# Kernel tuning notes

Measured on AMD Instinct MI355X. Metric: run time of the kernel, lower is better.

The kernel has to match this reference:

```python
import math
import jax, jax.numpy as jnp
import numpy as np

D_MODEL = 1024
H_HEADS = 16
D_K = D_MODEL // H_HEADS


def setup_inputs() -> dict:
    key = jax.random.key(0)
    ks = jax.random.split(key, 7)
    B, L = 4, 2048
    q = jax.random.normal(ks[0], (B, L, D_MODEL), dtype=jnp.float32)
    k = jax.random.normal(ks[1], (B, L, D_MODEL), dtype=jnp.float32)
    v = jax.random.normal(ks[2], (B, L, D_MODEL), dtype=jnp.float32)
    mask = jnp.ones((1, L, L), dtype=jnp.int32)
    # nn.Linear(d_model, d_model, bias=False) weights, shape (out, in)
    s = 1.0 / math.sqrt(D_MODEL)
    W_q = jax.random.uniform(ks[3], (D_MODEL, D_MODEL), jnp.float32, -s, s)
    W_k = jax.random.uniform(ks[4], (D_MODEL, D_MODEL), jnp.float32, -s, s)
    W_v = jax.random.uniform(ks[5], (D_MODEL, D_MODEL), jnp.float32, -s, s)
    W_o = jax.random.uniform(ks[6], (D_MODEL, D_MODEL), jnp.float32, -s, s)
    return {"q": q, "k": k, "v": v, "mask": mask,
            "W_q": W_q, "W_k": W_k, "W_v": W_v, "W_o": W_o}


def reference(q, k, v, mask, W_q, W_k, W_v, W_o):
    B, Lq, _ = q.shape
    # projections (Linear: x @ W.T) then split heads -> (B, H, L, d_k)
    def split_heads(x):
        return x.reshape(B, -1, H_HEADS, D_K).transpose(0, 2, 1, 3)
    Q = split_heads(jnp.einsum('bsd,ed->bse', q, W_q))
    K = split_heads(jnp.einsum('bsd,ed->bse', k, W_k))
    V = split_heads(jnp.einsum('bsd,ed->bse', v, W_v))
    # scores: (B, H, Lq, Lk)
    scores = jnp.einsum('bhqd,bhkd->bhqk', Q, K) / math.sqrt(D_K)
    m = mask[:, None, :, :]  # (1, 1, Lq, Lk) broadcast
    scores = jnp.where(m == 0, -jnp.inf, scores)
    weights = jax.nn.softmax(scores, axis=-1)
    attn = jnp.einsum('bhqk,bhkd->bhqd', weights, V)  # (B, H, Lq, d_v)
    attn = attn.transpose(0, 2, 1, 3).reshape(B, Lq, D_MODEL)
    return jnp.einsum('bse,de->bsd', attn, W_o)
```

## Files before the change

### kernel.cpp

```cpp
#include <hip/hip_runtime.h>
#include <hip/hip_bf16.h>


typedef unsigned short u16;
typedef float f32x4  __attribute__((ext_vector_type(4)));
typedef float f32x16 __attribute__((ext_vector_type(16)));
typedef short s16x8  __attribute__((ext_vector_type(8)));
typedef unsigned u32x4 __attribute__((ext_vector_type(4)));
typedef __bf16 bf16x8 __attribute__((ext_vector_type(8)));

#define QSCL 0.18033688011112042f

__device__ __forceinline__ u16 f2b(float f) {
    union { float f; unsigned u; } x; x.f = f;
    unsigned r = x.u + 0x7fffu + ((x.u >> 16) & 1u);
    return (u16)(r >> 16);
}

__device__ __forceinline__ f32x4 MF(s16x8 a, s16x8 b, f32x4 c) {
    return __builtin_amdgcn_mfma_f32_16x16x32_bf16(
        __builtin_bit_cast(bf16x8, a), __builtin_bit_cast(bf16x8, b), c, 0, 0, 0);
}
__device__ __forceinline__ f32x16 MF32(s16x8 a, s16x8 b, f32x16 c) {
    return __builtin_amdgcn_mfma_f32_32x32x16_bf16(
        __builtin_bit_cast(bf16x8, a), __builtin_bit_cast(bf16x8, b), c, 0, 0, 0);
}
__device__ __forceinline__ unsigned cvtpk(float lo, float hi) {
    unsigned r;
    asm("v_cvt_pk_bf16_f32 %0, %1, %2" : "=v"(r) : "v"(lo), "v"(hi));
    return r;
}
__device__ __forceinline__ void swap32(unsigned &a, unsigned &b) {
    asm volatile("v_permlane32_swap_b32 %0, %1" : "+v"(a), "+v"(b));
}
__device__ __forceinline__ float expa(float x) {
    float r;
    asm("v_exp_f32 %0, %1" : "=v"(r) : "v"(x));
    return r;
}
__device__ __forceinline__ void g2l16(const u16* g, u16* lbase) {
    __builtin_amdgcn_global_load_lds((const __attribute__((address_space(1))) void*)g,
                                     (__attribute__((address_space(3))) void*)lbase, 16, 0, 0);
}

__global__ __launch_bounds__(256)
void convert_and_mask(const float* __restrict__ q, const float* __restrict__ k,
                      const float* __restrict__ v, const float* __restrict__ Wq,
                      const float* __restrict__ Wk, const float* __restrict__ Wv,
                      const float* __restrict__ Wo, const int* __restrict__ mask,
                      u16* __restrict__ Abf, u16* __restrict__ Wbf,
                      int* __restrict__ mflag) {
    if (blockIdx.x < 256) {
        __shared__ int anyz;
        if (threadIdx.x == 0) anyz = 0;
        __syncthreads();
        const int qt = blockIdx.x >> 4, kt = blockIdx.x & 15;
        int local = 0;
#pragma unroll
        for (int qq = 0; qq < 16; ++qq) {
            int e4 = qq * 256 + threadIdx.x;
            int r = e4 >> 5, cc = (e4 & 31) * 4;
            int4 mv = *(const int4*)(mask + (size_t)(qt * 128 + r) * 2048 + kt * 128 + cc);
            local |= (mv.x == 0) | (mv.y == 0) | (mv.z == 0) | (mv.w == 0);
        }
        if (local) atomicOr(&anyz, 1);
        __syncthreads();
        if (threadIdx.x == 0) mflag[blockIdx.x] = anyz;
        return;
    }
    const size_t NQKV = 25165824;
    const size_t NCH  = 3670016;
    const size_t nconv = (size_t)(gridDim.x - 256) * 256;
    for (size_t cidx = (size_t)(blockIdx.x - 256) * 256 + threadIdx.x; cidx < NCH;
         cidx += nconv) {
        size_t e = cidx * 8;
        const float* src; u16* dst; float scl = 1.f;
        if (e < NQKV) {
            src = (e < 8388608) ? q + e
                : (e < 16777216) ? k + (e - 8388608) : v + (e - 16777216);
            dst = Abf + e;
        } else {
            size_t o = e - NQKV;
            if (o < 1048576)      { src = Wq + o; scl = QSCL; }
            else if (o < 2097152) { src = Wk + (o - 1048576); }
            else if (o < 3145728) { src = Wv + (o - 2097152); }
            else                  { src = Wo + (o - 3145728); }
            dst = Wbf + o;
        }
        float4 a = *(const float4*)(src);
        float4 b = *(const float4*)(src + 4);
        ushort4 p0, p1;
        p0.x = f2b(a.x * scl); p0.y = f2b(a.y * scl);
        p0.z = f2b(a.z * scl); p0.w = f2b(a.w * scl);
        p1.x = f2b(b.x * scl); p1.y = f2b(b.y * scl);
        p1.z = f2b(b.z * scl); p1.w = f2b(b.w * scl);
        *(ushort4*)dst = p0; *(ushort4*)(dst + 4) = p1;
    }
}

__global__ __launch_bounds__(256, 3)
void gemm_qkv_fast(const u16* __restrict__ Abf, const u16* __restrict__ Wbf,
                   u16* __restrict__ Qh, u16* __restrict__ Kf, u16* __restrict__ Vf) {
    __shared__ __align__(16) u16 As[128 * 32];
    __shared__ __align__(16) u16 Bs[128 * 32];
    const int z = blockIdx.z;
    const u16* A = Abf + (size_t)z * (8192 * 1024);
    const u16* W = Wbf + (size_t)z * (1024 * 1024);
    const int tid = threadIdx.x, l = tid & 63, w = tid >> 6;
    const int g = l >> 4, c = l & 15;
    const int m0 = blockIdx.x * 128, n0 = blockIdx.y * 128;
    const int wr = (w >> 1) * 64, wc = (w & 1) * 64;

    f32x4 acc[4][4];
#pragma unroll
    for (int i = 0; i < 4; ++i)
#pragma unroll
        for (int j = 0; j < 4; ++j)
#pragma unroll
            for (int e = 0; e < 4; ++e) acc[i][j][e] = 0.f;

    const u16* Ag = A + (size_t)(m0 + w * 32 + (l >> 2)) * 1024 + (l & 3) * 8;
    const u16* Wg = W + (size_t)(n0 + w * 32 + (l >> 2)) * 1024 + (l & 3) * 8;
    u16* Al = As + w * 1024;
    u16* Bl = Bs + w * 1024;

    for (int kt = 0; kt < 32; ++kt) {
        __syncthreads();
        g2l16(Ag + kt * 32,         Al);
        g2l16(Ag + kt * 32 + 16384, Al + 512);
        g2l16(Wg + kt * 32,         Bl);
        g2l16(Wg + kt * 32 + 16384, Bl + 512);
        __syncthreads();
        s16x8 af[4], bf[4];
#pragma unroll
        for (int i = 0; i < 4; ++i) {
            af[i] = *(const s16x8*)(As + (wr + i * 16 + c) * 32 + g * 8);
            bf[i] = *(const s16x8*)(Bs + (wc + i * 16 + c) * 32 + g * 8);
        }
#pragma unroll
        for (int mi = 0; mi < 4; ++mi)
#pragma unroll
            for (int ni = 0; ni < 4; ++ni)
                acc[mi][ni] = MF(af[mi], bf[ni], acc[mi][ni]);
    }

    if (z == 0) {
#pragma unroll
        for (int mi = 0; mi < 4; ++mi)
#pragma unroll
            for (int ni = 0; ni < 4; ++ni)
#pragma unroll
                for (int j = 0; j < 4; ++j) {
                    int row = m0 + wr + mi * 16 + g * 4 + j;
                    int col = n0 + wc + ni * 16 + c;
                    int b = row >> 11, sl = row & 2047;
                    int h = col >> 6, d = col & 63;
                    Qh[(((size_t)(b * 16 + h)) * 2048 + sl) * 64 + d] = f2b(acc[mi][ni][j]);
                }
    } else if (z == 1) {
#pragma unroll
        for (int mi = 0; mi < 4; ++mi)
#pragma unroll
            for (int ni = 0; ni < 4; ++ni)
#pragma unroll
                for (int j = 0; j < 4; ++j) {
                    int row = m0 + wr + mi * 16 + g * 4 + j;
                    int col = n0 + wc + ni * 16 + c;
                    int b = row >> 11, kk = row & 2047;
                    int h = col >> 6, d = col & 63;
                    size_t off = (size_t)(b * 16 + h) * 131072
                               + (size_t)(((kk >> 5) * 4 + (d >> 4))) * 512
                               + ((kk & 31) + 32 * ((d >> 3) & 1)) * 8 + (d & 7);
                    Kf[off] = f2b(acc[mi][ni][j]);
                }
    } else {
#pragma unroll
        for (int mi = 0; mi < 4; ++mi)
#pragma unroll
            for (int ni = 0; ni < 4; ++ni) {
                int key0 = m0 + wr + mi * 16 + g * 4;
                int col  = n0 + wc + ni * 16 + c;
                int b = key0 >> 11, kk0 = key0 & 2047;
                int h = col >> 6, d = col & 63;
                size_t off = (size_t)(b * 16 + h) * 131072
                           + (size_t)((kk0 >> 6) * 8 + (d >> 5) * 4 + ((kk0 >> 4) & 3)) * 512
                           + (((kk0 >> 3) & 1) * 32 + (d & 31)) * 8 + (kk0 & 7);
                ushort4 pk;
                pk.x = f2b(acc[mi][ni][0]); pk.y = f2b(acc[mi][ni][1]);
                pk.z = f2b(acc[mi][ni][2]); pk.w = f2b(acc[mi][ni][3]);
                *(ushort4*)(Vf + off) = pk;
            }
    }
}

__global__ __launch_bounds__(256, 3)
void gemm_out_fast(const u16* __restrict__ Ab, const u16* __restrict__ W,
                   float* __restrict__ Cout) {
    __shared__ __align__(16) u16 As[128 * 32];
    __shared__ __align__(16) u16 Bs[128 * 32];
    const int tid = threadIdx.x, l = tid & 63, w = tid >> 6;
    const int g = l >> 4, c = l & 15;
    const int m0 = blockIdx.x * 128, n0 = blockIdx.y * 128;
    const int wr = (w >> 1) * 64, wc = (w & 1) * 64;

    f32x4 acc[4][4];
#pragma unroll
    for (int i = 0; i < 4; ++i)
#pragma unroll
        for (int j = 0; j < 4; ++j)
#pragma unroll
            for (int e = 0; e < 4; ++e) acc[i][j][e] = 0.f;

    const u16* Ag = Ab + (size_t)(m0 + w * 32 + (l >> 2)) * 1024 + (l & 3) * 8;
    const u16* Wg = W  + (size_t)(n0 + w * 32 + (l >> 2)) * 1024 + (l & 3) * 8;
    u16* Al = As + w * 1024;
    u16* Bl = Bs + w * 1024;

    for (int kt = 0; kt < 32; ++kt) {
        __syncthreads();
        g2l16(Ag + kt * 32,         Al);
        g2l16(Ag + kt * 32 + 16384, Al + 512);
        g2l16(Wg + kt * 32,         Bl);
        g2l16(Wg + kt * 32 + 16384, Bl + 512);
        __syncthreads();
        s16x8 af[4], bf[4];
#pragma unroll
        for (int i = 0; i < 4; ++i) {
            af[i] = *(const s16x8*)(As + (wr + i * 16 + c) * 32 + g * 8);
            bf[i] = *(const s16x8*)(Bs + (wc + i * 16 + c) * 32 + g * 8);
        }
#pragma unroll
        for (int mi = 0; mi < 4; ++mi)
#pragma unroll
            for (int ni = 0; ni < 4; ++ni)
                acc[mi][ni] = MF(af[mi], bf[ni], acc[mi][ni]);
    }

#pragma unroll
    for (int mi = 0; mi < 4; ++mi)
#pragma unroll
        for (int ni = 0; ni < 4; ++ni)
#pragma unroll
            for (int j = 0; j < 4; ++j) {
                int row = m0 + wr + mi * 16 + g * 4 + j;
                int col = n0 + wc + ni * 16 + c;
                Cout[(size_t)row * 1024 + col] = acc[mi][ni][j];
            }
}

__global__ __launch_bounds__(512, 4)
void flash_attn(const u16* __restrict__ Qh, const u16* __restrict__ Kf,
                const u16* __restrict__ Vf, const int* __restrict__ mask,
                const int* __restrict__ mflag, u16* __restrict__ attnB) {
    __shared__ __align__(16) u16 KV[2][2][16][512];

    const int tid = threadIdx.x, w = tid >> 6, l = tid & 63;
    const int hi = l >> 5, q32 = l & 31;
    const int bh = blockIdx.x, qt = blockIdx.y;
    const size_t base = (size_t)bh * (2048 * 64);
    const u16* Qp = Qh + base;
    const u16* Kp = Kf + base;
    const u16* Vp = Vf + base;
    const int qrow_w = qt * 256 + w * 32;

    const int flagrow = qt * 2 + (w >> 2);
    int anyflag = 0;
#pragma unroll
    for (int i = 0; i < 16; ++i) anyflag |= mflag[flagrow * 16 + i];

    s16x8 Qf[4];
#pragma unroll
    for (int s = 0; s < 4; ++s)
        Qf[s] = *(const s16x8*)(Qp + (size_t)(qrow_w + q32) * 64 + s * 16 + hi * 8);

    s16x8 ones;
#pragma unroll
    for (int i = 0; i < 8; ++i) ones[i] = (short)0x3F80;

    f32x16 z16;
#pragma unroll
    for (int r = 0; r < 16; ++r) z16[r] = 0.f;
    f32x16 oA = z16, oB = z16, lacc = z16;

    auto stage = [&](int buf, int st) {
        const u16* ks = Kp + (size_t)(st * 16 + w * 2) * 512 + l * 8;
        const u16* vs = Vp + (size_t)(st * 16 + w * 2) * 512 + l * 8;
        g2l16(ks,       &KV[buf][0][w * 2][0]);
        g2l16(ks + 512, &KV[buf][0][w * 2 + 1][0]);
        g2l16(vs,       &KV[buf][1][w * 2][0]);
        g2l16(vs + 512, &KV[buf][1][w * 2 + 1][0]);
    };

    auto Shalf = [&](int buf, int h) -> f32x16 {
        const int rb = (h >> 1) * 8 + (h & 1) * 4;
        __builtin_amdgcn_s_setprio(1);
        s16x8 ka = *(const s16x8*)&KV[buf][0][rb][l * 8];
        f32x16 s = MF32(ka, Qf[0], z16);
#pragma unroll
        for (int ss = 1; ss < 4; ++ss) {
            ka = *(const s16x8*)&KV[buf][0][rb + ss][l * 8];
            s = MF32(ka, Qf[ss], s);
        }
        __builtin_amdgcn_s_setprio(0);
        return s;
    };
    auto expmask = [&](f32x16& s, int st, int h) {
        if (anyflag && mflag[flagrow * 16 + st] != 0) {
            const int qr = qrow_w + q32, kb = st * 128 + h * 32;
#pragma unroll
            for (int r = 0; r < 16; ++r) {
                int key = (r & 3) + 8 * (r >> 2) + 4 * hi;
                if (mask[(size_t)qr * 2048 + kb + key] == 0) s[r] = -1e30f;
            }
        }
#pragma unroll
        for (int r = 0; r < 16; ++r) s[r] = expa(s[r]);
    };
    auto packh = [&](const f32x16& s, s16x8& X0, s16x8& X1) {
        u32x4 t;
        unsigned a0 = cvtpk(s[0], s[1]),   a1 = cvtpk(s[2], s[3]);
        unsigned b0 = cvtpk(s[4], s[5]),   b1 = cvtpk(s[6], s[7]);
        swap32(a0, b0); swap32(a1, b1);
        t.x = a0; t.y = a1; t.z = b0; t.w = b1;
        X0 = __builtin_bit_cast(s16x8, t);
        unsigned c0 = cvtpk(s[8], s[9]),   c1 = cvtpk(s[10], s[11]);
        unsigned d0 = cvtpk(s[12], s[13]), d1 = cvtpk(s[14], s[15]);
        swap32(c0, d0); swap32(c1, d1);
        t.x = c0; t.y = c1; t.z = d0; t.w = d1;
        X1 = __builtin_bit_cast(s16x8, t);
    };
    auto PVhalf = [&](int buf, int h, s16x8 X0, s16x8 X1) {
        const int rb = (h >> 1) * 8, hb = (h & 1) * 2;
        __builtin_amdgcn_s_setprio(1);
        s16x8 v0 = *(const s16x8*)&KV[buf][1][rb + hb][l * 8];
        s16x8 v1 = *(const s16x8*)&KV[buf][1][rb + 4 + hb][l * 8];
        oA = MF32(X0, v0, oA);
        oB = MF32(X0, v1, oB);
        lacc = MF32(X0, ones, lacc);
        s16x8 v2 = *(const s16x8*)&KV[buf][1][rb + hb + 1][l * 8];
        s16x8 v3 = *(const s16x8*)&KV[buf][1][rb + 4 + hb + 1][l * 8];
        oA = MF32(X1, v2, oA);
        oB = MF32(X1, v3, oB);
        lacc = MF32(X1, ones, lacc);
        __builtin_amdgcn_s_setprio(0);
    };

    s16x8 Xc0, Xc1;

    auto processST = [&](int buf, int st) {
        f32x16 sp = Shalf(buf, 0);
        expmask(sp, st, 0);
#pragma unroll
        for (int h = 1; h < 4; ++h) {
            f32x16 sc = Shalf(buf, h);
            s16x8 Y0, Y1;
            packh(sp, Y0, Y1);
            PVhalf(buf, h - 1, Y0, Y1);
            expmask(sc, st, h);
            sp = sc;
        }
        packh(sp, Xc0, Xc1);
    };

    stage(0, 0);
    __syncthreads();
    stage(1, 1);
    processST(0, 0);

    for (int st = 1; st < 16; ++st) {
        const int buf = st & 1;
        PVhalf(buf ^ 1, 3, Xc0, Xc1);
        __syncthreads();
        if (st < 15) stage(buf ^ 1, st + 1);
        processST(buf, st);
    }
    PVhalf(1, 3, Xc0, Xc1);

    const int b = bh >> 4, h = bh & 15;
#pragma unroll
    for (int r = 0; r < 16; ++r) {
        int qloc = (r & 3) + 8 * (r >> 2) + 4 * hi;
        float inv = __builtin_amdgcn_rcpf(lacc[r]);
        int row = qrow_w + qloc;
        u16* dst = attnB + ((size_t)b * 2048 + row) * 1024 + h * 64 + q32;
        dst[0]  = f2b(oA[r] * inv);
        dst[32] = f2b(oB[r] * inv);
    }
}

extern "C" void kernel_launch(void* const* d_in, const int* in_sizes, int n_in,
                              void* d_out, int out_size, void* d_ws, size_t ws_size,
                              hipStream_t stream) {
    const float* q    = (const float*)d_in[0];
    const float* k    = (const float*)d_in[1];
    const float* v    = (const float*)d_in[2];
    const int*   mask = (const int*)d_in[3];
    const float* Wq   = (const float*)d_in[4];
    const float* Wk   = (const float*)d_in[5];
    const float* Wv   = (const float*)d_in[6];
    const float* Wo   = (const float*)d_in[7];

    char* ws = (char*)d_ws;
    u16* Abf   = (u16*)(ws);
    u16* Wbf   = (u16*)(ws + (48u << 20));
    u16* Qh    = (u16*)(ws + (56u << 20));
    u16* Kf    = (u16*)(ws + (72u << 20));
    u16* Vf    = (u16*)(ws + (88u << 20));
    u16* attnB = (u16*)(ws);
    int* mflag = (int*)(ws + (104u << 20));

    convert_and_mask<<<dim3(2304), dim3(256), 0, stream>>>(q, k, v, Wq, Wk, Wv, Wo,
                                                           mask, Abf, Wbf, mflag);
    gemm_qkv_fast<<<dim3(64, 8, 3), dim3(256), 0, stream>>>(Abf, Wbf, Qh, Kf, Vf);
    flash_attn<<<dim3(64, 8), dim3(512), 0, stream>>>(Qh, Kf, Vf, mask, mflag, attnB);
    gemm_out_fast<<<dim3(64, 8), dim3(256), 0, stream>>>(attnB, Wbf + 3145728, (float*)d_out);
}
```

Measured before the change: 192.1 us.

## Fuse fp32-to-bf16 conversion into projection GEMM tile loads

```diff
diff --git a/kernel.cpp b/kernel.cpp
--- a/kernel.cpp
+++ b/kernel.cpp
@@ -38,74 +38,46 @@
     asm("v_exp_f32 %0, %1" : "=v"(r) : "v"(x));
     return r;
 }
-__device__ __forceinline__ void g2l16(const u16* g, u16* lbase) {
+__device__ __forceinline__ void g2l16(const void* g, void* lbase) {
     __builtin_amdgcn_global_load_lds((const __attribute__((address_space(1))) void*)g,
                                      (__attribute__((address_space(3))) void*)lbase, 16, 0, 0);
 }
+__device__ __forceinline__ s16x8 pack8(f32x4 a, f32x4 b) {
+    u32x4 t;
+    t.x = cvtpk(a[0], a[1]); t.y = cvtpk(a[2], a[3]);
+    t.z = cvtpk(b[0], b[1]); t.w = cvtpk(b[2], b[3]);
+    return __builtin_bit_cast(s16x8, t);
+}
 
 __global__ __launch_bounds__(256)
-void convert_and_mask(const float* __restrict__ q, const float* __restrict__ k,
-                      const float* __restrict__ v, const float* __restrict__ Wq,
-                      const float* __restrict__ Wk, const float* __restrict__ Wv,
-                      const float* __restrict__ Wo, const int* __restrict__ mask,
-                      u16* __restrict__ Abf, u16* __restrict__ Wbf,
-                      int* __restrict__ mflag) {
-    if (blockIdx.x < 256) {
-        __shared__ int anyz;
-        if (threadIdx.x == 0) anyz = 0;
-        __syncthreads();
-        const int qt = blockIdx.x >> 4, kt = blockIdx.x & 15;
-        int local = 0;
-#pragma unroll
-        for (int qq = 0; qq < 16; ++qq) {
-            int e4 = qq * 256 + threadIdx.x;
-            int r = e4 >> 5, cc = (e4 & 31) * 4;
-            int4 mv = *(const int4*)(mask + (size_t)(qt * 128 + r) * 2048 + kt * 128 + cc);
-            local |= (mv.x == 0) | (mv.y == 0) | (mv.z == 0) | (mv.w == 0);
-        }
-        if (local) atomicOr(&anyz, 1);
-        __syncthreads();
-        if (threadIdx.x == 0) mflag[blockIdx.x] = anyz;
-        return;
-    }
-    const size_t NQKV = 25165824;
-    const size_t NCH  = 3670016;
-    const size_t nconv = (size_t)(gridDim.x - 256) * 256;
-    for (size_t cidx = (size_t)(blockIdx.x - 256) * 256 + threadIdx.x; cidx < NCH;
-         cidx += nconv) {
-        size_t e = cidx * 8;
-        const float* src; u16* dst; float scl = 1.f;
-        if (e < NQKV) {
-            src = (e < 8388608) ? q + e
-                : (e < 16777216) ? k + (e - 8388608) : v + (e - 16777216);
-            dst = Abf + e;
-        } else {
-            size_t o = e - NQKV;
-            if (o < 1048576)      { src = Wq + o; scl = QSCL; }
-            else if (o < 2097152) { src = Wk + (o - 1048576); }
-            else if (o < 3145728) { src = Wv + (o - 2097152); }
-            else                  { src = Wo + (o - 3145728); }
-            dst = Wbf + o;
-        }
-        float4 a = *(const float4*)(src);
-        float4 b = *(const float4*)(src + 4);
-        ushort4 p0, p1;
-        p0.x = f2b(a.x * scl); p0.y = f2b(a.y * scl);
-        p0.z = f2b(a.z * scl); p0.w = f2b(a.w * scl);
-        p1.x = f2b(b.x * scl); p1.y = f2b(b.y * scl);
-        p1.z = f2b(b.z * scl); p1.w = f2b(b.w * scl);
-        *(ushort4*)dst = p0; *(ushort4*)(dst + 4) = p1;
-    }
+void mask_flags(const int* __restrict__ mask, int* __restrict__ mflag) {
+    __shared__ int anyz;
+    if (threadIdx.x == 0) anyz = 0;
+    __syncthreads();
+    const int qt = blockIdx.x >> 4, kt = blockIdx.x & 15;
+    int local = 0;
+#pragma unroll
+    for (int qq = 0; qq < 16; ++qq) {
+        int e4 = qq * 256 + threadIdx.x;
+        int r = e4 >> 5, cc = (e4 & 31) * 4;
+        int4 mv = *(const int4*)(mask + (size_t)(qt * 128 + r) * 2048 + kt * 128 + cc);
+        local |= (mv.x == 0) | (mv.y == 0) | (mv.z == 0) | (mv.w == 0);
+    }
+    if (local) atomicOr(&anyz, 1);
+    __syncthreads();
+    if (threadIdx.x == 0) mflag[blockIdx.x] = anyz;
 }
 
 __global__ __launch_bounds__(256, 3)
-void gemm_qkv_fast(const u16* __restrict__ Abf, const u16* __restrict__ Wbf,
-                   u16* __restrict__ Qh, u16* __restrict__ Kf, u16* __restrict__ Vf) {
-    __shared__ __align__(16) u16 As[128 * 32];
-    __shared__ __align__(16) u16 Bs[128 * 32];
+void gemm_qkv_f32(const float* __restrict__ q, const float* __restrict__ k,
+                  const float* __restrict__ v, const float* __restrict__ Wq,
+                  const float* __restrict__ Wk, const float* __restrict__ Wv,
+                  u16* __restrict__ Qh, u16* __restrict__ Kf, u16* __restrict__ Vf) {
+    __shared__ __align__(16) float As[128 * 32];
+    __shared__ __align__(16) float Bs[128 * 32];
     const int z = blockIdx.z;
-    const u16* A = Abf + (size_t)z * (8192 * 1024);
-    const u16* W = Wbf + (size_t)z * (1024 * 1024);
+    const float* A = (z == 0) ? q : (z == 1) ? k : v;
+    const float* W = (z == 0) ? Wq : (z == 1) ? Wk : Wv;
     const int tid = threadIdx.x, l = tid & 63, w = tid >> 6;
     const int g = l >> 4, c = l & 15;
     const int m0 = blockIdx.x * 128, n0 = blockIdx.y * 128;
@@ -119,23 +91,33 @@
 #pragma unroll
             for (int e = 0; e < 4; ++e) acc[i][j][e] = 0.f;
 
-    const u16* Ag = A + (size_t)(m0 + w * 32 + (l >> 2)) * 1024 + (l & 3) * 8;
-    const u16* Wg = W + (size_t)(n0 + w * 32 + (l >> 2)) * 1024 + (l & 3) * 8;
-    u16* Al = As + w * 1024;
-    u16* Bl = Bs + w * 1024;
+    const int srow = w * 8 + (l >> 3);
+    const int scg  = ((l & 7) ^ (l >> 3)) * 4;
+    const float* Ag = A + (size_t)(m0 + srow) * 1024 + scg;
+    const float* Wg = W + (size_t)(n0 + srow) * 1024 + scg;
+    float* Al = As + w * 256;
+    float* Bl = Bs + w * 256;
 
     for (int kt = 0; kt < 32; ++kt) {
         __syncthreads();
-        g2l16(Ag + kt * 32,         Al);
-        g2l16(Ag + kt * 32 + 16384, Al + 512);
-        g2l16(Wg + kt * 32,         Bl);
-        g2l16(Wg + kt * 32 + 16384, Bl + 512);
+#pragma unroll
+        for (int i = 0; i < 4; ++i) {
+            g2l16(Ag + (size_t)i * 32768 + kt * 32, Al + i * 1024);
+            g2l16(Wg + (size_t)i * 32768 + kt * 32, Bl + i * 1024);
+        }
         __syncthreads();
         s16x8 af[4], bf[4];
+        const int x = c & 7;
 #pragma unroll
         for (int i = 0; i < 4; ++i) {
-            af[i] = *(const s16x8*)(As + (wr + i * 16 + c) * 32 + g * 8);
-            bf[i] = *(const s16x8*)(Bs + (wc + i * 16 + c) * 32 + g * 8);
+            int ra = (wr + i * 16 + c) * 32;
+            f32x4 a0 = *(const f32x4*)(As + ra + ((2 * g) ^ x) * 4);
+            f32x4 a1 = *(const f32x4*)(As + ra + ((2 * g + 1) ^ x) * 4);
+            af[i] = pack8(a0, a1);
+            int rb = (wc + i * 16 + c) * 32;
+            f32x4 b0 = *(const f32x4*)(Bs + rb + ((2 * g) ^ x) * 4);
+            f32x4 b1 = *(const f32x4*)(Bs + rb + ((2 * g + 1) ^ x) * 4);
+            bf[i] = pack8(b0, b1);
         }
 #pragma unroll
         for (int mi = 0; mi < 4; ++mi)
@@ -155,7 +137,8 @@
                     int col = n0 + wc + ni * 16 + c;
                     int b = row >> 11, sl = row & 2047;
                     int h = col >> 6, d = col & 63;
-                    Qh[(((size_t)(b * 16 + h)) * 2048 + sl) * 64 + d] = f2b(acc[mi][ni][j]);
+                    Qh[(((size_t)(b * 16 + h)) * 2048 + sl) * 64 + d] =
+                        f2b(acc[mi][ni][j] * QSCL);
                 }
     } else if (z == 1) {
 #pragma unroll
@@ -194,10 +177,10 @@
 }
 
 __global__ __launch_bounds__(256, 3)
-void gemm_out_fast(const u16* __restrict__ Ab, const u16* __restrict__ W,
-                   float* __restrict__ Cout) {
-    __shared__ __align__(16) u16 As[128 * 32];
-    __shared__ __align__(16) u16 Bs[128 * 32];
+void gemm_out_f32(const u16* __restrict__ Ab, const float* __restrict__ W,
+                  float* __restrict__ Cout) {
+    __shared__ __align__(16) u16   As[128 * 32];
+    __shared__ __align__(16) float Bs[128 * 32];
     const int tid = threadIdx.x, l = tid & 63, w = tid >> 6;
     const int g = l >> 4, c = l & 15;
     const int m0 = blockIdx.x * 128, n0 = blockIdx.y * 128;
@@ -212,22 +195,29 @@
             for (int e = 0; e < 4; ++e) acc[i][j][e] = 0.f;
 
     const u16* Ag = Ab + (size_t)(m0 + w * 32 + (l >> 2)) * 1024 + (l & 3) * 8;
-    const u16* Wg = W  + (size_t)(n0 + w * 32 + (l >> 2)) * 1024 + (l & 3) * 8;
     u16* Al = As + w * 1024;
-    u16* Bl = Bs + w * 1024;
+    const int srow = w * 8 + (l >> 3);
+    const int scg  = ((l & 7) ^ (l >> 3)) * 4;
+    const float* Wg = W + (size_t)(n0 + srow) * 1024 + scg;
+    float* Bl = Bs + w * 256;
 
     for (int kt = 0; kt < 32; ++kt) {
         __syncthreads();
         g2l16(Ag + kt * 32,         Al);
         g2l16(Ag + kt * 32 + 16384, Al + 512);
-        g2l16(Wg + kt * 32,         Bl);
-        g2l16(Wg + kt * 32 + 16384, Bl + 512);
+#pragma unroll
+        for (int i = 0; i < 4; ++i)
+            g2l16(Wg + (size_t)i * 32768 + kt * 32, Bl + i * 1024);
         __syncthreads();
         s16x8 af[4], bf[4];
+        const int x = c & 7;
 #pragma unroll
         for (int i = 0; i < 4; ++i) {
             af[i] = *(const s16x8*)(As + (wr + i * 16 + c) * 32 + g * 8);
-            bf[i] = *(const s16x8*)(Bs + (wc + i * 16 + c) * 32 + g * 8);
+            int rb = (wc + i * 16 + c) * 32;
+            f32x4 b0 = *(const f32x4*)(Bs + rb + ((2 * g) ^ x) * 4);
+            f32x4 b1 = *(const f32x4*)(Bs + rb + ((2 * g + 1) ^ x) * 4);
+            bf[i] = pack8(b0, b1);
         }
 #pragma unroll
         for (int mi = 0; mi < 4; ++mi)
@@ -401,17 +391,15 @@
     const float* Wo   = (const float*)d_in[7];
 
     char* ws = (char*)d_ws;
-    u16* Abf   = (u16*)(ws);
-    u16* Wbf   = (u16*)(ws + (48u << 20));
-    u16* Qh    = (u16*)(ws + (56u << 20));
-    u16* Kf    = (u16*)(ws + (72u << 20));
-    u16* Vf    = (u16*)(ws + (88u << 20));
-    u16* attnB = (u16*)(ws);
-    int* mflag = (int*)(ws + (104u << 20));
-
-    convert_and_mask<<<dim3(2304), dim3(256), 0, stream>>>(q, k, v, Wq, Wk, Wv, Wo,
-                                                           mask, Abf, Wbf, mflag);
-    gemm_qkv_fast<<<dim3(64, 8, 3), dim3(256), 0, stream>>>(Abf, Wbf, Qh, Kf, Vf);
+    u16* Qh    = (u16*)(ws);
+    u16* Kf    = (u16*)(ws + (16u << 20));
+    u16* Vf    = (u16*)(ws + (32u << 20));
+    u16* attnB = (u16*)(ws + (48u << 20));
+    int* mflag = (int*)(ws + (64u << 20));
+
+    mask_flags<<<dim3(256), dim3(256), 0, stream>>>(mask, mflag);
+    gemm_qkv_f32<<<dim3(64, 8, 3), dim3(256), 0, stream>>>(q, k, v, Wq, Wk, Wv,
+                                                           Qh, Kf, Vf);
     flash_attn<<<dim3(64, 8), dim3(512), 0, stream>>>(Qh, Kf, Vf, mask, mflag, attnB);
-    gemm_out_fast<<<dim3(64, 8), dim3(256), 0, stream>>>(attnB, Wbf + 3145728, (float*)d_out);
-}
+    gemm_out_f32<<<dim3(64, 8), dim3(256), 0, stream>>>(attnB, Wo, (float*)d_out);
+}
```

New measurement: 195.5 us. Within noise of the previous version (+1.8%).
